# Performance work log

Measured on AMD Instinct MI355X. Metric: run time of the kernel, lower is better.

## Reference

```python
import jax, jax.numpy as jnp
import numpy as np
from jax import lax

B, S, H, T = 64, 512, 1024, 21


def setup_inputs() -> dict:
    key = jax.random.key(0)
    k1, k2, k3, k4, k5, k6, k7 = jax.random.split(key, 7)
    hidden_states = jax.random.normal(k1, (B, S, H), dtype=jnp.float32)
    attention_mask = jnp.ones((B, S), dtype=jnp.int32)
    labels = jax.random.randint(k2, (B, S), 0, T).astype(jnp.int64)
    W = jax.random.normal(k3, (T, H), dtype=jnp.float32) * 0.02
    b = jnp.zeros((T,), dtype=jnp.float32)
    # torchcrf init: uniform(-0.1, 0.1)
    transitions = jax.random.uniform(k4, (T, T), minval=-0.1, maxval=0.1, dtype=jnp.float32)
    start_transitions = jax.random.uniform(k5, (T,), minval=-0.1, maxval=0.1, dtype=jnp.float32)
    end_transitions = jax.random.uniform(k6, (T,), minval=-0.1, maxval=0.1, dtype=jnp.float32)
    return {
        "hidden_states": hidden_states,
        "attention_mask": attention_mask,
        "labels": labels,
        "W": W,
        "b": b,
        "transitions": transitions,
        "start_transitions": start_transitions,
        "end_transitions": end_transitions,
    }


def _crf_log_likelihood(emissions, labels, mask, trans, start, end):
    # emissions [B,S,T], labels [B,S] int, mask [B,S] bool. reduction='sum'.
    Bn, Sn, Tn = emissions.shape
    maskf = mask.astype(emissions.dtype)
    emit_scores = jnp.take_along_axis(emissions, labels[:, :, None], axis=2)[:, :, 0]  # [B,S]
    trans_scores = trans[labels[:, :-1], labels[:, 1:]]  # [B,S-1]
    numerator = start[labels[:, 0]] + emit_scores[:, 0]
    numerator = numerator + jnp.sum((trans_scores + emit_scores[:, 1:]) * maskf[:, 1:], axis=1)
    seq_ends = jnp.sum(mask.astype(jnp.int32), axis=1) - 1  # [B]
    last_tags = labels[jnp.arange(Bn), seq_ends]
    numerator = numerator + end[last_tags]
    # partition via forward algorithm (scan over time)
    alpha0 = start[None, :] + emissions[:, 0]  # [B,T]
    def step(alpha, inp):
        emit_t, mask_t = inp  # [B,T], [B]
        nxt = jax.nn.logsumexp(alpha[:, :, None] + trans[None, :, :] + emit_t[:, None, :], axis=1)
        return jnp.where(mask_t[:, None], nxt, alpha), None
    alpha, _ = lax.scan(step, alpha0, (emissions[:, 1:].transpose(1, 0, 2), mask[:, 1:].T))
    log_Z = jax.nn.logsumexp(alpha + end[None, :], axis=1)  # [B]
    return jnp.sum(numerator - log_Z)


def _viterbi_decode(emissions, mask, trans, start, end):
    Bn, Sn, Tn = emissions.shape
    score0 = start[None, :] + emissions[:, 0]  # [B,T]
    identity_bp = jnp.broadcast_to(jnp.arange(Tn)[None, :], (Bn, Tn))
    def fwd(score, inp):
        emit_t, mask_t = inp
        broad = score[:, :, None] + trans[None, :, :]  # [B, prev, cur]
        best_prev = jnp.argmax(broad, axis=1)  # [B,T]
        nxt = jnp.max(broad, axis=1) + emit_t
        new_score = jnp.where(mask_t[:, None], nxt, score)
        bp = jnp.where(mask_t[:, None], best_prev, identity_bp)
        return new_score, bp
    final_score, bps = lax.scan(fwd, score0, (emissions[:, 1:].transpose(1, 0, 2), mask[:, 1:].T))
    last_tag = jnp.argmax(final_score + end[None, :], axis=1)  # [B] tag at pos S-1
    def back(tag, bp_t):
        prev = jnp.take_along_axis(bp_t, tag[:, None], axis=1)[:, 0]
        return prev, tag
    tag0, tags_rest = lax.scan(back, last_tag, bps, reverse=True)  # tags_rest[t] = tag at pos t+1
    tags = jnp.concatenate([tag0[None, :], tags_rest], axis=0).T  # [B,S]
    return jnp.where(mask, tags, 0).astype(jnp.int64)


def reference(hidden_states, attention_mask, labels, W, b, transitions, start_transitions, end_transitions):
    mask = attention_mask.astype(bool)
    # dropout is identity in eval mode
    emissions = jnp.einsum("bsh,th->bst", hidden_states, W) + b  # [B,S,T]
    log_prob = _crf_log_likelihood(emissions, labels, mask, transitions, start_transitions, end_transitions)
    loss = -log_prob
    pred = _viterbi_decode(emissions, mask, transitions, start_transitions, end_transitions)
    return loss, pred
```

## Files before the change

kernel.cpp:

```cpp
#include <hip/hip_runtime.h>
#include <math.h>
#include <stdint.h>

#define BB 64
#define SS 512
#define HH 1024
#define TT 21

template <int CTRL>
__device__ __forceinline__ float dpp_add(float v) {
  int t = __builtin_amdgcn_update_dpp(0, __float_as_int(v), CTRL, 0xF, 0xF, true);
  return v + __int_as_float(t);
}
__device__ __forceinline__ float wave_sum(float v) {
  v = dpp_add<0x121>(v);
  v = dpp_add<0x122>(v);
  v = dpp_add<0x124>(v);
  v = dpp_add<0x128>(v);
  v += __shfl_xor(v, 16);
  v += __shfl_xor(v, 32);
  return v;
}

#define DOT4(A, H, WV)    \
  A = fmaf(H.x, WV.x, A); \
  A = fmaf(H.y, WV.y, A); \
  A = fmaf(H.z, WV.z, A); \
  A = fmaf(H.w, WV.w, A)

__global__ __launch_bounds__(192, 4) void k_emis(const float* __restrict__ hs,
                                                 const float* __restrict__ W,
                                                 const float* __restrict__ bias,
                                                 float* __restrict__ emis) {
  __shared__ float part[192 * 14];
  const int tid = threadIdx.x;
  const int q = tid & 7;
  const int tmp = tid >> 3;
  const int tg = tmp % 3;
  const int rp = tmp / 3;
  const size_t row0 = (size_t)blockIdx.x * 16 + rp * 2;
  const float4* hp0 = (const float4*)(hs + row0 * HH);
  const float4* hp1 = (const float4*)(hs + (row0 + 1) * HH);
  const float* wb0 = W + (size_t)(tg * 7) * HH + q * 4;

  float a0[7] = {0.f, 0.f, 0.f, 0.f, 0.f, 0.f, 0.f};
  float a1[7] = {0.f, 0.f, 0.f, 0.f, 0.f, 0.f, 0.f};
  float4 h0 = hp0[q], h1 = hp1[q];
#pragma unroll 2
  for (int i = 0; i < 32; ++i) {
    const float4 hc0 = h0, hc1 = h1;
    if (i < 31) {
      h0 = hp0[(i + 1) * 8 + q];
      h1 = hp1[(i + 1) * 8 + q];
    }
    const float* wb = wb0 + (size_t)i * 32;
#pragma unroll
    for (int lt = 0; lt < 7; ++lt) {
      const float4 w = *(const float4*)(wb + (size_t)lt * HH);
      DOT4(a0[lt], hc0, w);
      DOT4(a1[lt], hc1, w);
    }
  }
#pragma unroll
  for (int lt = 0; lt < 7; ++lt) {
    part[tid * 14 + lt] = a0[lt];
    part[tid * 14 + 7 + lt] = a1[lt];
  }
  __syncthreads();

  for (int o = tid; o < 16 * TT; o += 192) {
    const int rr = o / TT;
    const int t = o - rr * TT;
    const int tg2 = t / 7;
    const int lt2 = t - tg2 * 7;
    const float* pp = part + (((rr >> 1) * 3 + tg2) * 8) * 14 + (rr & 1) * 7 + lt2;
    float s = ((pp[0] + pp[14]) + (pp[28] + pp[42])) +
              ((pp[56] + pp[70]) + (pp[84] + pp[98]));
    emis[(size_t)blockIdx.x * (16 * TT) + o] = s + bias[t];
  }
}

#define RLF(V, K) __int_as_float(__builtin_amdgcn_readlane(__float_as_int(V), K))

__global__ __launch_bounds__(64, 1) void k_scan(const float* __restrict__ emis,
                                                const int* __restrict__ mask,
                                                const float* __restrict__ trans,
                                                const float* __restrict__ sv,
                                                const float* __restrict__ ev,
                                                float* __restrict__ logZ,
                                                float* __restrict__ pred) {
  __shared__ float sE[SS * TT];
  __shared__ unsigned long long mb[9];
  __shared__ unsigned char bp[SS][32];
  __shared__ unsigned char sTag[SS];
  const int lane = threadIdx.x;
  const int j = lane;
  const bool act = (j < TT);
  const int jj = act ? j : 0;
  const int b = blockIdx.x & 63;

  {
    const float4* src = (const float4*)(emis + (size_t)b * SS * TT);
    float4* dst = (float4*)sE;
    for (int i = lane; i < SS * TT / 4; i += 64) dst[i] = src[i];
#pragma unroll
    for (int w = 0; w < 8; ++w) {
      unsigned long long bm = __ballot(mask[b * SS + w * 64 + lane] != 0);
      if (lane == 0) mb[w] = bm;
    }
    if (lane == 0) mb[8] = 0ull;
  }
  __syncthreads();

  if (blockIdx.x < 64) {
    float E[TT];
#pragma unroll
    for (int i = 0; i < TT; ++i) E[i] = __expf(trans[i * TT + jj]);
    float v = act ? __expf(sv[jj] + sE[jj]) : 0.f;
    float C = 0.f;
    float nxtv[8];
#pragma unroll
    for (int k = 0; k < 8; ++k) nxtv[k] = sE[(1 + k) * TT + jj];

#define CRF_STEP(P, SHB)                                                      \
  {                                                                           \
    const int mk = (int)((swin >> ((SHB) + (P))) & 1ull);                     \
    const float ge_t = ge[P];                                                 \
    const float v0 = RLF(v, 0), v1 = RLF(v, 1), v2 = RLF(v, 2);               \
    const float v3 = RLF(v, 3), v4 = RLF(v, 4), v5 = RLF(v, 5);               \
    const float v6 = RLF(v, 6), v7 = RLF(v, 7), v8 = RLF(v, 8);               \
    const float v9 = RLF(v, 9), v10 = RLF(v, 10), v11 = RLF(v, 11);           \
    const float v12 = RLF(v, 12), v13 = RLF(v, 13), v14 = RLF(v, 14);         \
    const float v15 = RLF(v, 15), v16 = RLF(v, 16), v17 = RLF(v, 17);         \
    const float v18 = RLF(v, 18), v19 = RLF(v, 19), v20 = RLF(v, 20);         \
    float scale = 1.0f;                                                       \
    if ((P) == 7) {                                                           \
      float m = fmaxf(fmaxf(fmaxf(v0, v1), fmaxf(v2, v3)),                    \
                      fmaxf(fmaxf(v4, v5), fmaxf(v6, v7)));                   \
      m = fmaxf(m, fmaxf(fmaxf(v8, v9), fmaxf(v10, v11)));                    \
      m = fmaxf(m, fmaxf(fmaxf(v12, v13), fmaxf(v14, v15)));                  \
      m = fmaxf(m, fmaxf(fmaxf(v16, v17), fmaxf(v18, v19)));                  \
      m = fmaxf(m, v20);                                                      \
      int ex = (int)((__float_as_uint(m) >> 23) & 255u) - 127;                \
      scale = __uint_as_float((unsigned)(127 - ex) << 23);                    \
      C += (float)ex * 0.6931471805599453f;                                   \
      v *= scale;                                                             \
    }                                                                         \
    float q0 = v0 * E[0], q1 = v1 * E[1], q2 = v2 * E[2];                     \
    q0 = fmaf(v3, E[3], q0);   q1 = fmaf(v4, E[4], q1);   q2 = fmaf(v5, E[5], q2);   \
    q0 = fmaf(v6, E[6], q0);   q1 = fmaf(v7, E[7], q1);   q2 = fmaf(v8, E[8], q2);   \
    q0 = fmaf(v9, E[9], q0);   q1 = fmaf(v10, E[10], q1); q2 = fmaf(v11, E[11], q2); \
    q0 = fmaf(v12, E[12], q0); q1 = fmaf(v13, E[13], q1); q2 = fmaf(v14, E[14], q2); \
    q0 = fmaf(v15, E[15], q0); q1 = fmaf(v16, E[16], q1); q2 = fmaf(v17, E[17], q2); \
    q0 = fmaf(v18, E[18], q0); q1 = fmaf(v19, E[19], q1); q2 = fmaf(v20, E[20], q2); \
    float vn = ((q0 + q1 + q2) * scale) * ge_t;                               \
    v = (act && mk) ? vn : v;                                                 \
  }

#pragma unroll 1
    for (int w = 0; w < 8; ++w) {
      const unsigned long long wa = mb[w], wb2 = mb[w + 1];
      const unsigned long long winv = (wa >> 1) | (wb2 << 63);
      const unsigned wlo = __builtin_amdgcn_readfirstlane((unsigned)winv);
      const unsigned whi = __builtin_amdgcn_readfirstlane((unsigned)(winv >> 32));
      const unsigned long long swin = ((unsigned long long)whi << 32) | wlo;
      const int nci = (w < 7) ? 8 : 7;
#pragma unroll 1
      for (int ci = 0; ci < nci; ++ci) {
        const int t0 = ((w << 3) + ci) * 8 + 1;
        float cur[8], ge[8];
#pragma unroll
        for (int k = 0; k < 8; ++k) cur[k] = nxtv[k];
#pragma unroll
        for (int k = 0; k < 8; ++k) ge[k] = __expf(cur[k]);
#pragma unroll
        for (int k = 0; k < 8; ++k) {
          int tl = t0 + 8 + k;
          tl = (tl < SS) ? tl : (SS - 1);
          nxtv[k] = sE[tl * TT + jj];
        }
        const int shb = ci << 3;
#pragma unroll
        for (int p = 0; p < 8; ++p) { CRF_STEP(p, shb); }
      }
      if (w == 7) {
        float cur[8], ge[8];
#pragma unroll
        for (int k = 0; k < 7; ++k) cur[k] = nxtv[k];
#pragma unroll
        for (int k = 0; k < 7; ++k) ge[k] = __expf(cur[k]);
#pragma unroll
        for (int p = 0; p < 7; ++p) { CRF_STEP(p, 56); }
      }
    }
#undef CRF_STEP
    float wv = act ? v * __expf(ev[jj]) : 0.f;
#pragma unroll
    for (int d = 32; d >= 1; d >>= 1) wv += __shfl_xor(wv, d);
    if (lane == 0) logZ[b] = C + __logf(wv);
  } else {
    float Tc[TT];
#pragma unroll
    for (int i = 0; i < TT; ++i) Tc[i] = trans[i * TT + jj];
    float sc = act ? (sv[jj] + sE[jj]) : -3.0e38f;
    float nxtv[8];
#pragma unroll
    for (int k = 0; k < 8; ++k) nxtv[k] = sE[(1 + k) * TT + jj];

#define ARGSTEP(BV, BI, VAL, IDX)          \
  {                                        \
    float x_ = (VAL) + Tc[IDX];            \
    if (x_ > BV) { BV = x_; BI = (IDX); }  \
  }
#define VIT_STEP(P, SHB, TCUR)                                                \
  {                                                                           \
    const int mk = (int)((swin >> ((SHB) + (P))) & 1ull);                     \
    const float e = cur[P];                                                   \
    const float s0 = RLF(sc, 0), s1 = RLF(sc, 1), s2 = RLF(sc, 2);            \
    const float s3 = RLF(sc, 3), s4 = RLF(sc, 4), s5 = RLF(sc, 5);            \
    const float s6 = RLF(sc, 6), s7 = RLF(sc, 7), s8 = RLF(sc, 8);            \
    const float s9 = RLF(sc, 9), s10 = RLF(sc, 10), s11 = RLF(sc, 11);        \
    const float s12 = RLF(sc, 12), s13 = RLF(sc, 13), s14 = RLF(sc, 14);      \
    const float s15 = RLF(sc, 15), s16 = RLF(sc, 16), s17 = RLF(sc, 17);      \
    const float s18 = RLF(sc, 18), s19 = RLF(sc, 19), s20 = RLF(sc, 20);      \
    float b0v, b1v, b2v;                                                      \
    int i0, i1, i2;                                                           \
    b0v = s0 + Tc[0]; i0 = 0;                                                 \
    b1v = s1 + Tc[1]; i1 = 1;                                                 \
    b2v = s2 + Tc[2]; i2 = 2;                                                 \
    ARGSTEP(b0v, i0, s3, 3);   ARGSTEP(b1v, i1, s4, 4);   ARGSTEP(b2v, i2, s5, 5);    \
    ARGSTEP(b0v, i0, s6, 6);   ARGSTEP(b1v, i1, s7, 7);   ARGSTEP(b2v, i2, s8, 8);    \
    ARGSTEP(b0v, i0, s9, 9);   ARGSTEP(b1v, i1, s10, 10); ARGSTEP(b2v, i2, s11, 11);  \
    ARGSTEP(b0v, i0, s12, 12); ARGSTEP(b1v, i1, s13, 13); ARGSTEP(b2v, i2, s14, 14);  \
    ARGSTEP(b0v, i0, s15, 15); ARGSTEP(b1v, i1, s16, 16); ARGSTEP(b2v, i2, s17, 17);  \
    ARGSTEP(b0v, i0, s18, 18); ARGSTEP(b1v, i1, s19, 19); ARGSTEP(b2v, i2, s20, 20);  \
    float best = b0v;                                                         \
    int bi = i0;                                                              \
    if (b1v > best || (b1v == best && i1 < bi)) { best = b1v; bi = i1; }      \
    if (b2v > best || (b2v == best && i2 < bi)) { best = b2v; bi = i2; }      \
    float ns = best + e;                                                      \
    sc = (act && mk) ? ns : sc;                                               \
    if (act) bp[TCUR][j] = (unsigned char)(mk ? bi : j);                      \
  }

#pragma unroll 1
    for (int w = 0; w < 8; ++w) {
      const unsigned long long wa = mb[w], wb2 = mb[w + 1];
      const unsigned long long winv = (wa >> 1) | (wb2 << 63);
      const unsigned wlo = __builtin_amdgcn_readfirstlane((unsigned)winv);
      const unsigned whi = __builtin_amdgcn_readfirstlane((unsigned)(winv >> 32));
      const unsigned long long swin = ((unsigned long long)whi << 32) | wlo;
      const int nci = (w < 7) ? 8 : 7;
#pragma unroll 1
      for (int ci = 0; ci < nci; ++ci) {
        const int t0 = ((w << 3) + ci) * 8 + 1;
        float cur[8];
#pragma unroll
        for (int k = 0; k < 8; ++k) cur[k] = nxtv[k];
#pragma unroll
        for (int k = 0; k < 8; ++k) {
          int tl = t0 + 8 + k;
          tl = (tl < SS) ? tl : (SS - 1);
          nxtv[k] = sE[tl * TT + jj];
        }
        const int shb = ci << 3;
#pragma unroll
        for (int p = 0; p < 8; ++p) { VIT_STEP(p, shb, t0 + p); }
      }
      if (w == 7) {
        float cur[8];
#pragma unroll
        for (int k = 0; k < 7; ++k) cur[k] = nxtv[k];
#pragma unroll
        for (int p = 0; p < 7; ++p) { VIT_STEP(p, 56, 505 + p); }
      }
    }
#undef VIT_STEP
#undef ARGSTEP
    float fsv = act ? (sc + ev[jj]) : -3.0e38f;
    int idx = j;
#pragma unroll
    for (int d = 32; d >= 1; d >>= 1) {
      float ov = __shfl_xor(fsv, d);
      int oi = __shfl_xor(idx, d);
      bool take = (ov > fsv) || (ov == fsv && oi < idx);
      fsv = take ? ov : fsv;
      idx = take ? oi : idx;
    }
    __syncthreads();
    if (lane == 0) {
      int tag = idx;
      sTag[SS - 1] = (unsigned char)tag;
      for (int t = SS - 1; t >= 1; --t) {
        tag = bp[t][tag];
        sTag[t - 1] = (unsigned char)tag;
      }
    }
    __syncthreads();
    for (int i = lane; i < SS; i += 64) {
      pred[(size_t)b * SS + i] = (float)(mask[b * SS + i] ? (int)sTag[i] : 0);
    }
  }
}

__global__ __launch_bounds__(64, 1) void k_loss(const float* __restrict__ emis,
                                                const int* __restrict__ mask,
                                                const int* __restrict__ labels,
                                                const float* __restrict__ trans,
                                                const float* __restrict__ sv,
                                                const float* __restrict__ ev,
                                                const float* __restrict__ logZ,
                                                float* __restrict__ outv) {
  const int b = blockIdx.x;
  const int lane = threadIdx.x;
  float p = 0.f;
  int cnt = 0;
  for (int t = lane; t < SS; t += 64) {
    cnt += mask[b * SS + t] ? 1 : 0;
    if (t >= 1) {
      const int lp = labels[b * SS + t - 1];
      const int lc = labels[b * SS + t];
      const float mk = (float)mask[b * SS + t];
      p += mk * (trans[lp * TT + lc] + emis[((size_t)b * SS + t) * TT + lc]);
    }
  }
  p = wave_sum(p);
#pragma unroll
  for (int d = 32; d >= 1; d >>= 1) cnt += __shfl_xor(cnt, d);
  if (lane == 0) {
    const int l0 = labels[b * SS];
    float numer = p + sv[l0] + emis[(size_t)b * SS * TT + l0];
    numer += ev[labels[b * SS + cnt - 1]];
    atomicAdd(outv, logZ[b] - numer);
  }
}

extern "C" void kernel_launch(void* const* d_in, const int* in_sizes, int n_in,
                              void* d_out, int out_size, void* d_ws, size_t ws_size,
                              hipStream_t stream) {
  const float* hs = (const float*)d_in[0];
  const int* msk = (const int*)d_in[1];
  const int* lab = (const int*)d_in[2];
  const float* W = (const float*)d_in[3];
  const float* bias = (const float*)d_in[4];
  const float* trans = (const float*)d_in[5];
  const float* sv = (const float*)d_in[6];
  const float* ev = (const float*)d_in[7];
  float* out = (float*)d_out;

  float* emis = (float*)d_ws;
  float* logZ = emis + (size_t)BB * SS * TT;

  hipMemsetAsync(d_out, 0, 4, stream);
  k_emis<<<2048, 192, 0, stream>>>(hs, W, bias, emis);
  k_scan<<<128, 64, 0, stream>>>(emis, msk, trans, sv, ev, logZ, out + 1);
  k_loss<<<64, 64, 0, stream>>>(emis, msk, lab, trans, sv, ev, logZ, out);
}
```

Baseline: 449.9 us.

## Fuse loss numerator into CRF forward kernel and split Viterbi into own kernel

```diff
diff --git a/kernel.cpp b/kernel.cpp
--- a/kernel.cpp
+++ b/kernel.cpp
@@ -82,22 +82,20 @@
 
 #define RLF(V, K) __int_as_float(__builtin_amdgcn_readlane(__float_as_int(V), K))
 
-__global__ __launch_bounds__(64, 1) void k_scan(const float* __restrict__ emis,
-                                                const int* __restrict__ mask,
-                                                const float* __restrict__ trans,
-                                                const float* __restrict__ sv,
-                                                const float* __restrict__ ev,
-                                                float* __restrict__ logZ,
-                                                float* __restrict__ pred) {
+__global__ __launch_bounds__(64, 1) void k_crf(const float* __restrict__ emis,
+                                               const int* __restrict__ mask,
+                                               const int* __restrict__ labels,
+                                               const float* __restrict__ trans,
+                                               const float* __restrict__ sv,
+                                               const float* __restrict__ ev,
+                                               float* __restrict__ outv) {
   __shared__ float sE[SS * TT];
   __shared__ unsigned long long mb[9];
-  __shared__ unsigned char bp[SS][32];
-  __shared__ unsigned char sTag[SS];
   const int lane = threadIdx.x;
   const int j = lane;
   const bool act = (j < TT);
   const int jj = act ? j : 0;
-  const int b = blockIdx.x & 63;
+  const int b = blockIdx.x;
 
   {
     const float4* src = (const float4*)(emis + (size_t)b * SS * TT);
@@ -112,15 +110,14 @@
   }
   __syncthreads();
 
-  if (blockIdx.x < 64) {
-    float E[TT];
-#pragma unroll
-    for (int i = 0; i < TT; ++i) E[i] = __expf(trans[i * TT + jj]);
-    float v = act ? __expf(sv[jj] + sE[jj]) : 0.f;
-    float C = 0.f;
-    float nxtv[8];
-#pragma unroll
-    for (int k = 0; k < 8; ++k) nxtv[k] = sE[(1 + k) * TT + jj];
+  float E[TT];
+#pragma unroll
+  for (int i = 0; i < TT; ++i) E[i] = __expf(trans[i * TT + jj]);
+  float v = act ? __expf(sv[jj] + sE[jj]) : 0.f;
+  float C = 0.f;
+  float nxtv[8];
+#pragma unroll
+  for (int k = 0; k < 8; ++k) nxtv[k] = sE[(1 + k) * TT + jj];
 
 #define CRF_STEP(P, SHB)                                                      \
   {                                                                           \
@@ -158,54 +155,105 @@
   }
 
 #pragma unroll 1
+  for (int w = 0; w < 8; ++w) {
+    const unsigned long long wa = mb[w], wb2 = mb[w + 1];
+    const unsigned long long winv = (wa >> 1) | (wb2 << 63);
+    const unsigned wlo = __builtin_amdgcn_readfirstlane((unsigned)winv);
+    const unsigned whi = __builtin_amdgcn_readfirstlane((unsigned)(winv >> 32));
+    const unsigned long long swin = ((unsigned long long)whi << 32) | wlo;
+    const int nci = (w < 7) ? 8 : 7;
+#pragma unroll 1
+    for (int ci = 0; ci < nci; ++ci) {
+      const int t0 = ((w << 3) + ci) * 8 + 1;
+      float cur[8], ge[8];
+#pragma unroll
+      for (int k = 0; k < 8; ++k) cur[k] = nxtv[k];
+#pragma unroll
+      for (int k = 0; k < 8; ++k) ge[k] = __expf(cur[k]);
+#pragma unroll
+      for (int k = 0; k < 8; ++k) {
+        int tl = t0 + 8 + k;
+        tl = (tl < SS) ? tl : (SS - 1);
+        nxtv[k] = sE[tl * TT + jj];
+      }
+      const int shb = ci << 3;
+#pragma unroll
+      for (int p = 0; p < 8; ++p) { CRF_STEP(p, shb); }
+    }
+    if (w == 7) {
+      float cur[8], ge[8];
+#pragma unroll
+      for (int k = 0; k < 7; ++k) cur[k] = nxtv[k];
+#pragma unroll
+      for (int k = 0; k < 7; ++k) ge[k] = __expf(cur[k]);
+#pragma unroll
+      for (int p = 0; p < 7; ++p) { CRF_STEP(p, 56); }
+    }
+  }
+#undef CRF_STEP
+  float wv = act ? v * __expf(ev[jj]) : 0.f;
+#pragma unroll
+  for (int d = 32; d >= 1; d >>= 1) wv += __shfl_xor(wv, d);
+  const float logZv = C + __logf(wv);
+
+  int cnt = 0;
+#pragma unroll
+  for (int w = 0; w < 8; ++w) cnt += (int)__popcll(mb[w]);
+  const int* lab = labels + b * SS;
+  float p = 0.f;
+  for (int t = lane; t < SS; t += 64) {
+    if (t >= 1) {
+      const int lp = lab[t - 1];
+      const int lc = lab[t];
+      const float mk = (float)((mb[t >> 6] >> (t & 63)) & 1ull);
+      p += mk * (trans[lp * TT + lc] + sE[t * TT + lc]);
+    }
+  }
+  p = wave_sum(p);
+  if (lane == 0) {
+    const int l0 = lab[0];
+    float numer = p + sv[l0] + sE[l0];
+    numer += ev[lab[cnt - 1]];
+    atomicAdd(outv, logZv - numer);
+  }
+}
+
+__global__ __launch_bounds__(64, 1) void k_vit(const float* __restrict__ emis,
+                                               const int* __restrict__ mask,
+                                               const float* __restrict__ trans,
+                                               const float* __restrict__ sv,
+                                               const float* __restrict__ ev,
+                                               float* __restrict__ pred) {
+  __shared__ float sE[SS * TT];
+  __shared__ unsigned long long mb[9];
+  __shared__ unsigned char bp[SS][32];
+  __shared__ unsigned char sTag[SS];
+  const int lane = threadIdx.x;
+  const int j = lane;
+  const bool act = (j < TT);
+  const int jj = act ? j : 0;
+  const int b = blockIdx.x;
+
+  {
+    const float4* src = (const float4*)(emis + (size_t)b * SS * TT);
+    float4* dst = (float4*)sE;
+    for (int i = lane; i < SS * TT / 4; i += 64) dst[i] = src[i];
+#pragma unroll
     for (int w = 0; w < 8; ++w) {
-      const unsigned long long wa = mb[w], wb2 = mb[w + 1];
-      const unsigned long long winv = (wa >> 1) | (wb2 << 63);
-      const unsigned wlo = __builtin_amdgcn_readfirstlane((unsigned)winv);
-      const unsigned whi = __builtin_amdgcn_readfirstlane((unsigned)(winv >> 32));
-      const unsigned long long swin = ((unsigned long long)whi << 32) | wlo;
-      const int nci = (w < 7) ? 8 : 7;
-#pragma unroll 1
-      for (int ci = 0; ci < nci; ++ci) {
-        const int t0 = ((w << 3) + ci) * 8 + 1;
-        float cur[8], ge[8];
-#pragma unroll
-        for (int k = 0; k < 8; ++k) cur[k] = nxtv[k];
-#pragma unroll
-        for (int k = 0; k < 8; ++k) ge[k] = __expf(cur[k]);
-#pragma unroll
-        for (int k = 0; k < 8; ++k) {
-          int tl = t0 + 8 + k;
-          tl = (tl < SS) ? tl : (SS - 1);
-          nxtv[k] = sE[tl * TT + jj];
-        }
-        const int shb = ci << 3;
-#pragma unroll
-        for (int p = 0; p < 8; ++p) { CRF_STEP(p, shb); }
-      }
-      if (w == 7) {
-        float cur[8], ge[8];
-#pragma unroll
-        for (int k = 0; k < 7; ++k) cur[k] = nxtv[k];
-#pragma unroll
-        for (int k = 0; k < 7; ++k) ge[k] = __expf(cur[k]);
-#pragma unroll
-        for (int p = 0; p < 7; ++p) { CRF_STEP(p, 56); }
-      }
-    }
-#undef CRF_STEP
-    float wv = act ? v * __expf(ev[jj]) : 0.f;
-#pragma unroll
-    for (int d = 32; d >= 1; d >>= 1) wv += __shfl_xor(wv, d);
-    if (lane == 0) logZ[b] = C + __logf(wv);
-  } else {
-    float Tc[TT];
-#pragma unroll
-    for (int i = 0; i < TT; ++i) Tc[i] = trans[i * TT + jj];
-    float sc = act ? (sv[jj] + sE[jj]) : -3.0e38f;
-    float nxtv[8];
-#pragma unroll
-    for (int k = 0; k < 8; ++k) nxtv[k] = sE[(1 + k) * TT + jj];
+      unsigned long long bm = __ballot(mask[b * SS + w * 64 + lane] != 0);
+      if (lane == 0) mb[w] = bm;
+    }
+    if (lane == 0) mb[8] = 0ull;
+  }
+  __syncthreads();
+
+  float Tc[TT];
+#pragma unroll
+  for (int i = 0; i < TT; ++i) Tc[i] = trans[i * TT + jj];
+  float sc = act ? (sv[jj] + sE[jj]) : -3.0e38f;
+  float nxtv[8];
+#pragma unroll
+  for (int k = 0; k < 8; ++k) nxtv[k] = sE[(1 + k) * TT + jj];
 
 #define ARGSTEP(BV, BI, VAL, IDX)          \
   {                                        \
@@ -244,94 +292,61 @@
   }
 
 #pragma unroll 1
-    for (int w = 0; w < 8; ++w) {
-      const unsigned long long wa = mb[w], wb2 = mb[w + 1];
-      const unsigned long long winv = (wa >> 1) | (wb2 << 63);
-      const unsigned wlo = __builtin_amdgcn_readfirstlane((unsigned)winv);
-      const unsigned whi = __builtin_amdgcn_readfirstlane((unsigned)(winv >> 32));
-      const unsigned long long swin = ((unsigned long long)whi << 32) | wlo;
-      const int nci = (w < 7) ? 8 : 7;
+  for (int w = 0; w < 8; ++w) {
+    const unsigned long long wa = mb[w], wb2 = mb[w + 1];
+    const unsigned long long winv = (wa >> 1) | (wb2 << 63);
+    const unsigned wlo = __builtin_amdgcn_readfirstlane((unsigned)winv);
+    const unsigned whi = __builtin_amdgcn_readfirstlane((unsigned)(winv >> 32));
+    const unsigned long long swin = ((unsigned long long)whi << 32) | wlo;
+    const int nci = (w < 7) ? 8 : 7;
 #pragma unroll 1
-      for (int ci = 0; ci < nci; ++ci) {
-        const int t0 = ((w << 3) + ci) * 8 + 1;
-        float cur[8];
-#pragma unroll
-        for (int k = 0; k < 8; ++k) cur[k] = nxtv[k];
-#pragma unroll
-        for (int k = 0; k < 8; ++k) {
-          int tl = t0 + 8 + k;
-          tl = (tl < SS) ? tl : (SS - 1);
-          nxtv[k] = sE[tl * TT + jj];
-        }
-        const int shb = ci << 3;
-#pragma unroll
-        for (int p = 0; p < 8; ++p) { VIT_STEP(p, shb, t0 + p); }
+    for (int ci = 0; ci < nci; ++ci) {
+      const int t0 = ((w << 3) + ci) * 8 + 1;
+      float cur[8];
+#pragma unroll
+      for (int k = 0; k < 8; ++k) cur[k] = nxtv[k];
+#pragma unroll
+      for (int k = 0; k < 8; ++k) {
+        int tl = t0 + 8 + k;
+        tl = (tl < SS) ? tl : (SS - 1);
+        nxtv[k] = sE[tl * TT + jj];
       }
-      if (w == 7) {
-        float cur[8];
-#pragma unroll
-        for (int k = 0; k < 7; ++k) cur[k] = nxtv[k];
-#pragma unroll
-        for (int p = 0; p < 7; ++p) { VIT_STEP(p, 56, 505 + p); }
-      }
-    }
+      const int shb = ci << 3;
+#pragma unroll
+      for (int p = 0; p < 8; ++p) { VIT_STEP(p, shb, t0 + p); }
+    }
+    if (w == 7) {
+      float cur[8];
+#pragma unroll
+      for (int k = 0; k < 7; ++k) cur[k] = nxtv[k];
+#pragma unroll
+      for (int p = 0; p < 7; ++p) { VIT_STEP(p, 56, 505 + p); }
+    }
+  }
 #undef VIT_STEP
 #undef ARGSTEP
-    float fsv = act ? (sc + ev[jj]) : -3.0e38f;
-    int idx = j;
-#pragma unroll
-    for (int d = 32; d >= 1; d >>= 1) {
-      float ov = __shfl_xor(fsv, d);
-      int oi = __shfl_xor(idx, d);
-      bool take = (ov > fsv) || (ov == fsv && oi < idx);
-      fsv = take ? ov : fsv;
-      idx = take ? oi : idx;
-    }
-    __syncthreads();
-    if (lane == 0) {
-      int tag = idx;
-      sTag[SS - 1] = (unsigned char)tag;
-      for (int t = SS - 1; t >= 1; --t) {
-        tag = bp[t][tag];
-        sTag[t - 1] = (unsigned char)tag;
-      }
-    }
-    __syncthreads();
-    for (int i = lane; i < SS; i += 64) {
-      pred[(size_t)b * SS + i] = (float)(mask[b * SS + i] ? (int)sTag[i] : 0);
-    }
-  }
-}
-
-__global__ __launch_bounds__(64, 1) void k_loss(const float* __restrict__ emis,
-                                                const int* __restrict__ mask,
-                                                const int* __restrict__ labels,
-                                                const float* __restrict__ trans,
-                                                const float* __restrict__ sv,
-                                                const float* __restrict__ ev,
-                                                const float* __restrict__ logZ,
-                                                float* __restrict__ outv) {
-  const int b = blockIdx.x;
-  const int lane = threadIdx.x;
-  float p = 0.f;
-  int cnt = 0;
-  for (int t = lane; t < SS; t += 64) {
-    cnt += mask[b * SS + t] ? 1 : 0;
-    if (t >= 1) {
-      const int lp = labels[b * SS + t - 1];
-      const int lc = labels[b * SS + t];
-      const float mk = (float)mask[b * SS + t];
-      p += mk * (trans[lp * TT + lc] + emis[((size_t)b * SS + t) * TT + lc]);
-    }
-  }
-  p = wave_sum(p);
-#pragma unroll
-  for (int d = 32; d >= 1; d >>= 1) cnt += __shfl_xor(cnt, d);
+  float fsv = act ? (sc + ev[jj]) : -3.0e38f;
+  int idx = j;
+#pragma unroll
+  for (int d = 32; d >= 1; d >>= 1) {
+    float ov = __shfl_xor(fsv, d);
+    int oi = __shfl_xor(idx, d);
+    bool take = (ov > fsv) || (ov == fsv && oi < idx);
+    fsv = take ? ov : fsv;
+    idx = take ? oi : idx;
+  }
+  __syncthreads();
   if (lane == 0) {
-    const int l0 = labels[b * SS];
-    float numer = p + sv[l0] + emis[(size_t)b * SS * TT + l0];
-    numer += ev[labels[b * SS + cnt - 1]];
-    atomicAdd(outv, logZ[b] - numer);
+    int tag = idx;
+    sTag[SS - 1] = (unsigned char)tag;
+    for (int t = SS - 1; t >= 1; --t) {
+      tag = bp[t][tag];
+      sTag[t - 1] = (unsigned char)tag;
+    }
+  }
+  __syncthreads();
+  for (int i = lane; i < SS; i += 64) {
+    pred[(size_t)b * SS + i] = (float)(mask[b * SS + i] ? (int)sTag[i] : 0);
   }
 }
 
@@ -349,10 +364,9 @@
   float* out = (float*)d_out;
 
   float* emis = (float*)d_ws;
-  float* logZ = emis + (size_t)BB * SS * TT;
 
   hipMemsetAsync(d_out, 0, 4, stream);
   k_emis<<<2048, 192, 0, stream>>>(hs, W, bias, emis);
-  k_scan<<<128, 64, 0, stream>>>(emis, msk, trans, sv, ev, logZ, out + 1);
-  k_loss<<<64, 64, 0, stream>>>(emis, msk, lab, trans, sv, ev, logZ, out);
-}
+  k_crf<<<64, 64, 0, stream>>>(emis, msk, lab, trans, sv, ev, out);
+  k_vit<<<64, 64, 0, stream>>>(emis, msk, trans, sv, ev, out + 1);
+}
```

Measured after the change: 516.1 us. 1.15x slower.
